# Performance work log

Hardware: AMD Instinct MI355X
Metric: run time of the kernel (lower is better)

## Reference

```python
import jax, jax.numpy as jnp
import numpy as np

F_CONST = 1.0
B_CONST = 0.1
R_CONST = 0.01
N, DIM = 8192, 64


def setup_inputs() -> dict:
    key = jax.random.key(0)
    k1, k2 = jax.random.split(key)
    x = jax.random.uniform(k1, (N, DIM), dtype=jnp.float32)
    A = jax.random.uniform(k2, (N, N), dtype=jnp.float32)
    return {"t": 0, "x": x, "A": A}


def reference(t, x, A):
    # dx_i/dt = f - b*x_i - diag(A @ (r * x x^T))
    # diag(A @ (x x^T))[i] = sum_j A_ij <x_j, x_i> = <x_i, (A x)_i>
    Ax = A @ x                                      # [N, DIM]
    outer = R_CONST * jnp.sum(x * Ax, axis=1, keepdims=True)  # [N, 1]
    return F_CONST - B_CONST * x - outer            # broadcasts to [N, DIM]
```

## Files before the change

### kernel.cpp

```cpp
#include <hip/hip_runtime.h>

#define N 8192
#define DIM 64

typedef float f32x4 __attribute__((ext_vector_type(4)));
typedef short bf16x8 __attribute__((ext_vector_type(8)));

__device__ __forceinline__ unsigned short f32_to_bf16_rne(float f) {
  unsigned int u = __float_as_uint(f);
  unsigned int r = (u + 0x7FFFu + ((u >> 16) & 1u)) >> 16;
  return (unsigned short)r;
}

__global__ void cvt_kernel(const float* __restrict__ x, unsigned short* __restrict__ xb) {
  int gid = blockIdx.x * blockDim.x + threadIdx.x;
  float4 v = reinterpret_cast<const float4*>(x)[gid];
  ushort4 o;
  o.x = f32_to_bf16_rne(v.x);
  o.y = f32_to_bf16_rne(v.y);
  o.z = f32_to_bf16_rne(v.z);
  o.w = f32_to_bf16_rne(v.w);
  reinterpret_cast<ushort4*>(xb)[gid] = o;
}

__global__ __launch_bounds__(256, 4) void main_kernel(
    const float* __restrict__ A,
    const unsigned short* __restrict__ xb,
    float* __restrict__ spart) {
  int bid = blockIdx.x;
  int rg = bid & 127;
  int js = bid >> 7;
  int tid = threadIdx.x;
  int w = tid >> 6;
  int lane = tid & 63;
  int i0w = rg * 64 + w * 16;
  int jbase = js * 1024;
  int c = lane & 15;
  int q = lane >> 4;
  int h = lane >> 5;
  int m = lane & 31;

  __shared__ alignas(16) float G[4][16][132];

  const unsigned short* pxi = xb + (size_t)(i0w + c) * DIM + q * 8;
  bf16x8 xi0 = *reinterpret_cast<const bf16x8*>(pxi);
  bf16x8 xi1 = *reinterpret_cast<const bf16x8*>(pxi + 32);

  float sacc[8] = {0.f, 0.f, 0.f, 0.f, 0.f, 0.f, 0.f, 0.f};
  f32x4 a_buf[8];

  const float* pA = A + (size_t)(i0w + h) * N + jbase + m * 4;

#pragma unroll
  for (int a = 0; a < 8; ++a)
    a_buf[a] = *reinterpret_cast<const f32x4*>(pA + (size_t)(a * 2) * N);

  for (int cc = 0; cc < 8; ++cc) {
    int jc = jbase + cc * 128;

#pragma unroll
    for (int jt = 0; jt < 8; ++jt) {
      const unsigned short* pj = xb + (size_t)(jc + jt * 16 + c) * DIM + q * 8;
      bf16x8 xj0 = *reinterpret_cast<const bf16x8*>(pj);
      bf16x8 xj1 = *reinterpret_cast<const bf16x8*>(pj + 32);
      f32x4 g = {0.f, 0.f, 0.f, 0.f};
      g = __builtin_amdgcn_mfma_f32_16x16x32_bf16(xj0, xi0, g, 0, 0, 0);
      g = __builtin_amdgcn_mfma_f32_16x16x32_bf16(xj1, xi1, g, 0, 0, 0);
      *reinterpret_cast<f32x4*>(&G[w][c][jt * 16 + q * 4]) = g;
    }

#pragma unroll
    for (int a = 0; a < 8; ++a) {
      f32x4 g4 = *reinterpret_cast<const f32x4*>(&G[w][a * 2 + h][m * 4]);
      f32x4 a4 = a_buf[a];
      float s = sacc[a];
      s = fmaf(a4[0], g4[0], s);
      s = fmaf(a4[1], g4[1], s);
      s = fmaf(a4[2], g4[2], s);
      s = fmaf(a4[3], g4[3], s);
      sacc[a] = s;
    }

    if (cc < 7) {
      const float* pAn = pA + (cc + 1) * 128;
#pragma unroll
      for (int a = 0; a < 8; ++a)
        a_buf[a] = *reinterpret_cast<const f32x4*>(pAn + (size_t)(a * 2) * N);
    }
  }

#pragma unroll
  for (int a = 0; a < 8; ++a) {
    float s = sacc[a];
    s += __shfl_xor(s, 1);
    s += __shfl_xor(s, 2);
    s += __shfl_xor(s, 4);
    s += __shfl_xor(s, 8);
    s += __shfl_xor(s, 16);
    sacc[a] = s;
  }
  if (m == 0) {
#pragma unroll
    for (int a = 0; a < 8; ++a)
      spart[(size_t)js * N + i0w + a * 2 + h] = sacc[a];
  }
}

__global__ void finish_kernel(const float* __restrict__ x,
                              const float* __restrict__ spart,
                              float* __restrict__ out) {
  int gid = blockIdx.x * blockDim.x + threadIdx.x;
  float4 xv = reinterpret_cast<const float4*>(x)[gid];
  int i = gid >> 4;
  float s = 0.f;
#pragma unroll
  for (int cc = 0; cc < 8; ++cc) s += spart[(size_t)cc * N + i];
  float4 o;
  o.x = 1.0f - 0.1f * xv.x - 0.01f * s;
  o.y = 1.0f - 0.1f * xv.y - 0.01f * s;
  o.z = 1.0f - 0.1f * xv.z - 0.01f * s;
  o.w = 1.0f - 0.1f * xv.w - 0.01f * s;
  reinterpret_cast<float4*>(out)[gid] = o;
}

extern "C" void kernel_launch(void* const* d_in, const int* in_sizes, int n_in,
                              void* d_out, int out_size, void* d_ws, size_t ws_size,
                              hipStream_t stream) {
  const float* x = (const float*)d_in[1];
  const float* A = (const float*)d_in[2];
  float* out = (float*)d_out;

  unsigned short* xb = (unsigned short*)d_ws;
  float* spart = (float*)((char*)d_ws + (size_t)N * DIM * 2);

  cvt_kernel<<<512, 256, 0, stream>>>(x, xb);
  main_kernel<<<1024, 256, 0, stream>>>(A, xb, spart);
  finish_kernel<<<512, 256, 0, stream>>>(x, spart, out);
}
```

Measured before the change: 83.71 us.

## Fuse finish into main kernel, drop LDS Gram staging, use MFMA-layout A loads

Restructures the main kernel so each 512-thread block owns 16 rows, with 8 waves splitting the j range. A is loaded directly in the MFMA output layout, so the Gram tile no longer needs an LDS round trip. The partial sums are reduced in shared memory within the block and the output is written there, which removes the finish kernel and the partial-sum buffer. The change also double-buffers the A and x_j loads in registers and maps blocks to XCDs so neighbouring row groups share an L2. Each lane now reads A in 16-byte pieces strided across 16 rows, which may hurt coalescing compared with the previous row-contiguous reads.

```diff
diff --git a/kernel.cpp b/kernel.cpp
--- a/kernel.cpp
+++ b/kernel.cpp
@@ -23,104 +23,90 @@
   reinterpret_cast<ushort4*>(xb)[gid] = o;
 }
 
-__global__ __launch_bounds__(256, 4) void main_kernel(
+__global__ __launch_bounds__(512, 4) void main_kernel(
     const float* __restrict__ A,
     const unsigned short* __restrict__ xb,
-    float* __restrict__ spart) {
+    const float* __restrict__ x,
+    float* __restrict__ out) {
   int bid = blockIdx.x;
-  int rg = bid & 127;
-  int js = bid >> 7;
+  int xcd = bid & 7;
+  int slot = bid >> 3;
+  int rg = xcd * 64 + slot;
+  int i0 = rg * 16;
   int tid = threadIdx.x;
   int w = tid >> 6;
   int lane = tid & 63;
-  int i0w = rg * 64 + w * 16;
-  int jbase = js * 1024;
   int c = lane & 15;
   int q = lane >> 4;
-  int h = lane >> 5;
-  int m = lane & 31;
+  int jbase = w * 1024;
 
-  __shared__ alignas(16) float G[4][16][132];
-
-  const unsigned short* pxi = xb + (size_t)(i0w + c) * DIM + q * 8;
+  const unsigned short* pxi = xb + (size_t)(i0 + c) * DIM + q * 8;
   bf16x8 xi0 = *reinterpret_cast<const bf16x8*>(pxi);
   bf16x8 xi1 = *reinterpret_cast<const bf16x8*>(pxi + 32);
 
-  float sacc[8] = {0.f, 0.f, 0.f, 0.f, 0.f, 0.f, 0.f, 0.f};
-  f32x4 a_buf[8];
+  const float* pA = A + (size_t)(i0 + c) * N + jbase + q * 4;
+  const unsigned short* pXJ = xb + (size_t)(jbase + c) * DIM + q * 8;
 
-  const float* pA = A + (size_t)(i0w + h) * N + jbase + m * 4;
+  float sacc = 0.f;
+
+  f32x4 a_buf[2][4];
+  bf16x8 xj_buf[2][4][2];
 
 #pragma unroll
-  for (int a = 0; a < 8; ++a)
-    a_buf[a] = *reinterpret_cast<const f32x4*>(pA + (size_t)(a * 2) * N);
-
-  for (int cc = 0; cc < 8; ++cc) {
-    int jc = jbase + cc * 128;
+  for (int u = 0; u < 4; ++u) {
+    a_buf[0][u] = *reinterpret_cast<const f32x4*>(pA + u * 16);
+    const unsigned short* pj = pXJ + (size_t)(u * 16) * DIM;
+    xj_buf[0][u][0] = *reinterpret_cast<const bf16x8*>(pj);
+    xj_buf[0][u][1] = *reinterpret_cast<const bf16x8*>(pj + 32);
+  }
 
 #pragma unroll
-    for (int jt = 0; jt < 8; ++jt) {
-      const unsigned short* pj = xb + (size_t)(jc + jt * 16 + c) * DIM + q * 8;
-      bf16x8 xj0 = *reinterpret_cast<const bf16x8*>(pj);
-      bf16x8 xj1 = *reinterpret_cast<const bf16x8*>(pj + 32);
+  for (int jg = 0; jg < 16; ++jg) {
+    const int cur = jg & 1, nxt = cur ^ 1;
+    if (jg < 15) {
+#pragma unroll
+      for (int u = 0; u < 4; ++u) {
+        int jt = (jg + 1) * 4 + u;
+        a_buf[nxt][u] = *reinterpret_cast<const f32x4*>(pA + jt * 16);
+        const unsigned short* pj = pXJ + (size_t)(jt * 16) * DIM;
+        xj_buf[nxt][u][0] = *reinterpret_cast<const bf16x8*>(pj);
+        xj_buf[nxt][u][1] = *reinterpret_cast<const bf16x8*>(pj + 32);
+      }
+    }
+#pragma unroll
+    for (int u = 0; u < 4; ++u) {
       f32x4 g = {0.f, 0.f, 0.f, 0.f};
-      g = __builtin_amdgcn_mfma_f32_16x16x32_bf16(xj0, xi0, g, 0, 0, 0);
-      g = __builtin_amdgcn_mfma_f32_16x16x32_bf16(xj1, xi1, g, 0, 0, 0);
-      *reinterpret_cast<f32x4*>(&G[w][c][jt * 16 + q * 4]) = g;
-    }
-
-#pragma unroll
-    for (int a = 0; a < 8; ++a) {
-      f32x4 g4 = *reinterpret_cast<const f32x4*>(&G[w][a * 2 + h][m * 4]);
-      f32x4 a4 = a_buf[a];
-      float s = sacc[a];
-      s = fmaf(a4[0], g4[0], s);
-      s = fmaf(a4[1], g4[1], s);
-      s = fmaf(a4[2], g4[2], s);
-      s = fmaf(a4[3], g4[3], s);
-      sacc[a] = s;
-    }
-
-    if (cc < 7) {
-      const float* pAn = pA + (cc + 1) * 128;
-#pragma unroll
-      for (int a = 0; a < 8; ++a)
-        a_buf[a] = *reinterpret_cast<const f32x4*>(pAn + (size_t)(a * 2) * N);
+      g = __builtin_amdgcn_mfma_f32_16x16x32_bf16(xj_buf[cur][u][0], xi0, g, 0, 0, 0);
+      g = __builtin_amdgcn_mfma_f32_16x16x32_bf16(xj_buf[cur][u][1], xi1, g, 0, 0, 0);
+      f32x4 a4 = a_buf[cur][u];
+      sacc = fmaf(a4[0], g[0], sacc);
+      sacc = fmaf(a4[1], g[1], sacc);
+      sacc = fmaf(a4[2], g[2], sacc);
+      sacc = fmaf(a4[3], g[3], sacc);
     }
   }
 
+  sacc += __shfl_xor(sacc, 16);
+  sacc += __shfl_xor(sacc, 32);
+
+  __shared__ float red[8][16];
+  if (lane < 16) red[w][lane] = sacc;
+  __syncthreads();
+
+  if (tid < 256) {
+    int r = tid >> 4, cq = tid & 15;
+    float s = 0.f;
 #pragma unroll
-  for (int a = 0; a < 8; ++a) {
-    float s = sacc[a];
-    s += __shfl_xor(s, 1);
-    s += __shfl_xor(s, 2);
-    s += __shfl_xor(s, 4);
-    s += __shfl_xor(s, 8);
-    s += __shfl_xor(s, 16);
-    sacc[a] = s;
+    for (int ww = 0; ww < 8; ++ww) s += red[ww][r];
+    int i = i0 + r;
+    f32x4 xv = *reinterpret_cast<const f32x4*>(x + (size_t)i * DIM + cq * 4);
+    f32x4 o;
+    o[0] = 1.0f - 0.1f * xv[0] - 0.01f * s;
+    o[1] = 1.0f - 0.1f * xv[1] - 0.01f * s;
+    o[2] = 1.0f - 0.1f * xv[2] - 0.01f * s;
+    o[3] = 1.0f - 0.1f * xv[3] - 0.01f * s;
+    *reinterpret_cast<f32x4*>(out + (size_t)i * DIM + cq * 4) = o;
   }
-  if (m == 0) {
-#pragma unroll
-    for (int a = 0; a < 8; ++a)
-      spart[(size_t)js * N + i0w + a * 2 + h] = sacc[a];
-  }
-}
-
-__global__ void finish_kernel(const float* __restrict__ x,
-                              const float* __restrict__ spart,
-                              float* __restrict__ out) {
-  int gid = blockIdx.x * blockDim.x + threadIdx.x;
-  float4 xv = reinterpret_cast<const float4*>(x)[gid];
-  int i = gid >> 4;
-  float s = 0.f;
-#pragma unroll
-  for (int cc = 0; cc < 8; ++cc) s += spart[(size_t)cc * N + i];
-  float4 o;
-  o.x = 1.0f - 0.1f * xv.x - 0.01f * s;
-  o.y = 1.0f - 0.1f * xv.y - 0.01f * s;
-  o.z = 1.0f - 0.1f * xv.z - 0.01f * s;
-  o.w = 1.0f - 0.1f * xv.w - 0.01f * s;
-  reinterpret_cast<float4*>(out)[gid] = o;
 }
 
 extern "C" void kernel_launch(void* const* d_in, const int* in_sizes, int n_in,
@@ -131,9 +117,7 @@
   float* out = (float*)d_out;
 
   unsigned short* xb = (unsigned short*)d_ws;
-  float* spart = (float*)((char*)d_ws + (size_t)N * DIM * 2);
 
   cvt_kernel<<<512, 256, 0, stream>>>(x, xb);
-  main_kernel<<<1024, 256, 0, stream>>>(A, xb, spart);
-  finish_kernel<<<512, 256, 0, stream>>>(x, spart, out);
+  main_kernel<<<512, 512, 0, stream>>>(A, xb, x, out);
 }
```

Measured after the change: 103.9 us. 1.24x slower.
